# Kernel tuning notes

Measured on AMD Instinct MI355X. Metric: run time of the kernel, lower is better.

## Reference

```python
import jax, jax.numpy as jnp
import numpy as np

N, E, F_IN, HID, HEADS, CLASSES = 50000, 800000, 128, 128, 4, 2
NEG_SLOPE = 0.2


def _gatv2_layer(x, Wl, Wr, att, bias, src, dst, heads, concat):
    # PyG GATv2Conv (share_weights=False, eval mode):
    #   e_ij = att . leaky_relu(Wl x_j + Wr x_i); alpha = segment_softmax over dst;
    #   out_i = sum_j alpha_ij * (Wl x_j)
    n = x.shape[0]
    c = att.shape[-1]
    xl = (x @ Wl).reshape(n, heads, c)   # source transform [N,H,C]
    xr = (x @ Wr).reshape(n, heads, c)   # target transform [N,H,C]
    e = jax.nn.leaky_relu(xl[src] + xr[dst], NEG_SLOPE)      # [E,H,C]
    logits = jnp.einsum('ehc,hc->eh', e, att)                # [E,H]
    m = jax.ops.segment_max(logits, dst, num_segments=n)     # stable softmax per dst
    p = jnp.exp(logits - m[dst])
    denom = jax.ops.segment_sum(p, dst, num_segments=n)
    alpha = p / (denom[dst] + 1e-16)                         # [E,H]
    out = jax.ops.segment_sum(alpha[:, :, None] * xl[src], dst, num_segments=n)  # [N,H,C]
    out = out.reshape(n, heads * c) if concat else out.mean(axis=1)
    return out + bias


def setup_inputs() -> dict:
    key = jax.random.key(0)
    ks = jax.random.split(key, 16)
    s = lambda fan_in: 1.0 / np.sqrt(fan_in)
    inp = {
        'x': jax.random.normal(ks[0], (N, F_IN), jnp.float32),
        'edge_idx': jax.random.randint(ks[1], (2, E), 0, N, jnp.int64),
        'w_in': jax.random.normal(ks[2], (F_IN, HID), jnp.float32) * s(F_IN),
        'b_in': jnp.zeros((HID,), jnp.float32),
        'wl1': jax.random.normal(ks[3], (HID, HEADS * HID), jnp.float32) * s(HID),
        'wr1': jax.random.normal(ks[4], (HID, HEADS * HID), jnp.float32) * s(HID),
        'att1': jax.random.normal(ks[5], (HEADS, HID), jnp.float32) * s(HID),
        'b1': jnp.zeros((HEADS * HID,), jnp.float32),
        'wl2': jax.random.normal(ks[6], (HEADS * HID, HID), jnp.float32) * s(HEADS * HID),
        'wr2': jax.random.normal(ks[7], (HEADS * HID, HID), jnp.float32) * s(HEADS * HID),
        'att2': jax.random.normal(ks[8], (1, HID), jnp.float32) * s(HID),
        'b2': jnp.zeros((HID,), jnp.float32),
        'w_out': jax.random.normal(ks[9], (HID, CLASSES), jnp.float32) * s(HID),
        'b_out': jnp.zeros((CLASSES,), jnp.float32),
    }
    return inp


def reference(x, edge_idx, w_in, b_in, wl1, wr1, att1, b1, wl2, wr2, att2, b2, w_out, b_out):
    n = x.shape[0]
    loops = jnp.arange(n, dtype=edge_idx.dtype)  # PyG add_self_loops=True
    src = jnp.concatenate([edge_idx[0], loops])
    dst = jnp.concatenate([edge_idx[1], loops])
    h = jax.nn.elu(x @ w_in + b_in)              # dropout is identity in eval
    h = jax.nn.elu(_gatv2_layer(h, wl1, wr1, att1, b1, src, dst, HEADS, True))
    h = jax.nn.elu(_gatv2_layer(h, wl2, wr2, att2, b2, src, dst, 1, False))
    logits = h @ w_out + b_out
    return jax.nn.log_softmax(logits, axis=1)
```

## Files before the change

### kernel.cpp

```cpp
#include <hip/hip_runtime.h>
#include <hip/hip_bf16.h>
#include <math.h>

#define F_IN   128
#define HID    128
#define HEADS  4
#define HC1    (HEADS*HID)
#define CLASSES 2
#define NEG_SLOPE 0.2f
#define LOG2E 1.44269504088896340736f
#define MNEG  -3.0e38f

#define SCAN_CHUNK 2048

typedef __attribute__((ext_vector_type(8))) short short8;
typedef __attribute__((ext_vector_type(4))) float f32x4;
typedef __attribute__((ext_vector_type(2))) float f32x2;

__device__ __forceinline__ f32x2 unpack2(unsigned u) {
    f32x2 r;
    r.x = __uint_as_float(u << 16);
    r.y = __uint_as_float(u & 0xffff0000u);
    return r;
}

__global__ void zero_int_kernel(int* __restrict__ p, int n) {
    int i = blockIdx.x * blockDim.x + threadIdx.x;
    int stride = gridDim.x * blockDim.x;
    for (; i < n; i += stride) p[i] = 0;
}

__global__ void deg_kernel(const int* __restrict__ dst_arr, int* __restrict__ deg,
                           int E, int N) {
    int e = blockIdx.x * blockDim.x + threadIdx.x;
    if (e >= E) return;
    int d = dst_arr[e];
    if ((unsigned)d >= (unsigned)N) d = 0;
    atomicAdd(&deg[d], 1);
}

__global__ void scan_partial_kernel(const int* __restrict__ deg, int* __restrict__ bsum, int n) {
    __shared__ int sdata[256];
    int b = blockIdx.x, t = threadIdx.x;
    int base = b * SCAN_CHUNK;
    int s = 0;
    for (int i = t; i < SCAN_CHUNK; i += 256) {
        int idx = base + i;
        s += (idx < n) ? deg[idx] : 0;
    }
    sdata[t] = s;
    __syncthreads();
    for (int off = 128; off; off >>= 1) {
        if (t < off) sdata[t] += sdata[t + off];
        __syncthreads();
    }
    if (t == 0) bsum[b] = sdata[0];
}

__global__ void scan_bsums_kernel(int* __restrict__ bsum, int nb, int* __restrict__ row, int n) {
    if (blockIdx.x == 0 && threadIdx.x == 0) {
        int acc = 0;
        for (int i = 0; i < nb; ++i) { int v = bsum[i]; bsum[i] = acc; acc += v; }
        row[n] = acc;
    }
}

__global__ void scan_final_kernel(const int* __restrict__ deg, const int* __restrict__ bsum,
                                  int* __restrict__ row, int* __restrict__ cursor, int n) {
    __shared__ int tsum[256];
    int b = blockIdx.x, t = threadIdx.x;
    int base = b * SCAN_CHUNK + t * 8;
    int local[8];
    int s = 0;
    #pragma unroll
    for (int k = 0; k < 8; ++k) {
        int idx = base + k;
        int v = (idx < n) ? deg[idx] : 0;
        local[k] = s;
        s += v;
    }
    tsum[t] = s;
    __syncthreads();
    for (int off = 1; off < 256; off <<= 1) {
        int v = 0;
        if (t >= off) v = tsum[t - off];
        __syncthreads();
        if (t >= off) tsum[t] += v;
        __syncthreads();
    }
    int texcl = (t == 0) ? 0 : tsum[t - 1];
    int boff = bsum[b];
    #pragma unroll
    for (int k = 0; k < 8; ++k) {
        int idx = base + k;
        if (idx < n) {
            int v = boff + texcl + local[k];
            row[idx] = v;
            cursor[idx] = v;
        }
    }
}

__global__ void scatter_kernel(const int* __restrict__ src_arr, const int* __restrict__ dst_arr,
                               int* __restrict__ cursor, int* __restrict__ src_sorted,
                               int E, int N) {
    int e = blockIdx.x * blockDim.x + threadIdx.x;
    if (e >= E) return;
    int s = src_arr[e], d = dst_arr[e];
    if ((unsigned)s >= (unsigned)N) s = 0;
    if ((unsigned)d >= (unsigned)N) d = 0;
    int pos = atomicAdd(&cursor[d], 1);
    src_sorted[pos] = s;
}

__global__ void weights_prep_kernel(
    const float* __restrict__ w_in, const float* __restrict__ wl1,
    const float* __restrict__ wr1, const float* __restrict__ wl2,
    const float* __restrict__ wr2,
    __hip_bfloat16* __restrict__ w_inT, __hip_bfloat16* __restrict__ wT1,
    __hip_bfloat16* __restrict__ wT2)
{
    int t = blockIdx.x * blockDim.x + threadIdx.x;
    const int S0 = 128 * 128, S1 = 128 * 512;
    if (t < S0) {
        int n = t / 128, k = t % 128;
        w_inT[t] = __float2bfloat16(w_in[(size_t)k * 128 + n]);
    } else if (t < S0 + S1) {
        int idx = t - S0;
        int n = idx / 128, k = idx % 128;
        wT1[idx] = __float2bfloat16(wl1[(size_t)k * 512 + n]);
    } else if (t < S0 + 2 * S1) {
        int idx = t - S0 - S1;
        int n = idx / 128, k = idx % 128;
        wT1[(size_t)(512 + n) * 128 + k] = __float2bfloat16(wr1[(size_t)k * 512 + n]);
    } else if (t < S0 + 3 * S1) {
        int idx = t - S0 - 2 * S1;
        int n = idx / 512, k = idx % 512;
        wT2[idx] = __float2bfloat16(wl2[(size_t)k * 128 + n]);
    } else if (t < S0 + 4 * S1) {
        int idx = t - S0 - 3 * S1;
        int n = idx / 512, k = idx % 512;
        wT2[(size_t)(128 + n) * 512 + k] = __float2bfloat16(wr2[(size_t)k * 128 + n]);
    }
}

template<int ACT, typename AT, typename OutT>
__global__ __launch_bounds__(256) void mfma_gemm_kernel(
    const AT* __restrict__ A,
    const __hip_bfloat16* __restrict__ BT,
    const float* __restrict__ bias,
    OutT* __restrict__ C,
    int M, int K, int N)
{
    constexpr int BM = 128, BN = 128, BK = 64, LDA = 72;
    __shared__ __align__(16) short As[BM * LDA];
    __shared__ __align__(16) short Bs[BN * LDA];

    const int tid  = threadIdx.x;
    const int lane = tid & 63;
    const int wid  = tid >> 6;
    const int wm   = wid >> 1;
    const int wn   = wid & 1;
    const int fr   = lane & 15;
    const int fk   = (lane >> 4) * 8;

    const int row0 = blockIdx.y * BM;
    const int col0 = blockIdx.x * BN;

    const short* Bg = (const short*)BT;

    f32x4 acc[4][4] = {};

    for (int k0 = 0; k0 < K; k0 += BK) {
        #pragma unroll
        for (int it = 0; it < 4; ++it) {
            int chunk = it * 256 + tid;
            int r = chunk >> 3, c = chunk & 7;
            int gr = row0 + r;
            short8 v = {0, 0, 0, 0, 0, 0, 0, 0};
            if (gr < M) {
                if constexpr (sizeof(AT) == 2) {
                    v = *(const short8*)((const short*)A + (size_t)gr * K + k0 + c * 8);
                } else {
                    const float* ap = (const float*)A + (size_t)gr * K + k0 + c * 8;
                    float4 a0 = *(const float4*)ap;
                    float4 a1 = *(const float4*)(ap + 4);
                    __hip_bfloat16 h;
                    h = __float2bfloat16(a0.x); v[0] = *(short*)&h;
                    h = __float2bfloat16(a0.y); v[1] = *(short*)&h;
                    h = __float2bfloat16(a0.z); v[2] = *(short*)&h;
                    h = __float2bfloat16(a0.w); v[3] = *(short*)&h;
                    h = __float2bfloat16(a1.x); v[4] = *(short*)&h;
                    h = __float2bfloat16(a1.y); v[5] = *(short*)&h;
                    h = __float2bfloat16(a1.z); v[6] = *(short*)&h;
                    h = __float2bfloat16(a1.w); v[7] = *(short*)&h;
                }
            }
            *(short8*)(&As[r * LDA + c * 8]) = v;
        }
        #pragma unroll
        for (int it = 0; it < 4; ++it) {
            int chunk = it * 256 + tid;
            int n = chunk >> 3, c = chunk & 7;
            short8 v = *(const short8*)(Bg + (size_t)(col0 + n) * K + k0 + c * 8);
            *(short8*)(&Bs[n * LDA + c * 8]) = v;
        }
        __syncthreads();
        #pragma unroll
        for (int kk = 0; kk < 2; ++kk) {
            short8 af[4], bf[4];
            #pragma unroll
            for (int i = 0; i < 4; ++i)
                af[i] = *(const short8*)(&As[(wm * 64 + i * 16 + fr) * LDA + kk * 32 + fk]);
            #pragma unroll
            for (int j = 0; j < 4; ++j)
                bf[j] = *(const short8*)(&Bs[(wn * 64 + j * 16 + fr) * LDA + kk * 32 + fk]);
            #pragma unroll
            for (int i = 0; i < 4; ++i)
                #pragma unroll
                for (int j = 0; j < 4; ++j)
                    acc[i][j] = __builtin_amdgcn_mfma_f32_16x16x32_bf16(af[i], bf[j], acc[i][j], 0, 0, 0);
        }
        __syncthreads();
    }

    const int crow = row0 + wm * 64;
    const int ccol = col0 + wn * 64;
    #pragma unroll
    for (int i = 0; i < 4; ++i) {
        #pragma unroll
        for (int j = 0; j < 4; ++j) {
            int col = ccol + j * 16 + (lane & 15);
            float bv = bias ? bias[col] : 0.0f;
            #pragma unroll
            for (int reg = 0; reg < 4; ++reg) {
                int r = crow + i * 16 + (lane >> 4) * 4 + reg;
                if (r < M) {
                    float v = acc[i][j][reg] + bv;
                    if (ACT == 1) v = (v > 0.0f) ? v : expm1f(v);
                    C[(size_t)r * N + col] = (OutT)v;
                }
            }
        }
    }
}

__global__ __launch_bounds__(256) void gatv2_l1_fused_kernel(
    const __hip_bfloat16* __restrict__ xlr,
    const int* __restrict__ row, const int* __restrict__ src_sorted,
    const float* __restrict__ att, const float* __restrict__ b1,
    __hip_bfloat16* __restrict__ out1, int N)
{
    int d = blockIdx.x * 4 + (threadIdx.x >> 6);
    if (d >= N) return;
    int lane = threadIdx.x & 63;
    int cbase = lane * 8;
    const short* basep = (const short*)xlr;

    f32x2 xrd2[4], attv2[4];
    {
        uint4 raw = *reinterpret_cast<const uint4*>(basep + (size_t)d * 1024 + 512 + cbase);
        const unsigned* u = reinterpret_cast<const unsigned*>(&raw);
        #pragma unroll
        for (int j = 0; j < 4; ++j) xrd2[j] = unpack2(u[j]);
        #pragma unroll
        for (int j = 0; j < 4; ++j) {
            attv2[j].x = att[cbase + 2 * j] * LOG2E;
            attv2[j].y = att[cbase + 2 * j + 1] * LOG2E;
        }
    }

    float m = MNEG;
    float s = 0.0f;
    f32x2 o2[4] = {};

    int rs = row[d], re = row[d + 1];

    uint4 raw = *reinterpret_cast<const uint4*>(basep + (size_t)d * 1024 + cbase);
    for (int it = rs - 1; it < re; ++it) {
        uint4 cur = raw;
        if (it + 1 < re) {
            int sn = src_sorted[it + 1];
            raw = *reinterpret_cast<const uint4*>(basep + (size_t)sn * 1024 + cbase);
        }
        const unsigned* u = reinterpret_cast<const unsigned*>(&cur);
        f32x2 v2[4];
        #pragma unroll
        for (int j = 0; j < 4; ++j) v2[j] = unpack2(u[j]);

        f32x2 tacc = {0.0f, 0.0f};
        #pragma unroll
        for (int j = 0; j < 4; ++j) {
            f32x2 e = v2[j] + xrd2[j];
            f32x2 ne = e * NEG_SLOPE;
            e.x = fmaxf(e.x, ne.x);
            e.y = fmaxf(e.y, ne.y);
            tacc = __builtin_elementwise_fma(e, attv2[j], tacc);
        }
        float t = tacc.x + tacc.y;
        t += __shfl_xor(t, 1);
        t += __shfl_xor(t, 2);
        t += __shfl_xor(t, 4);
        t += __shfl_xor(t, 8);
        if (t > m) {
            float r = exp2f(m - t);
            s *= r;
            f32x2 r2 = {r, r};
            #pragma unroll
            for (int j = 0; j < 4; ++j) o2[j] *= r2;
            m = t;
        }
        float p = exp2f(t - m);
        s += p;
        f32x2 p2 = {p, p};
        #pragma unroll
        for (int j = 0; j < 4; ++j) o2[j] = __builtin_elementwise_fma(p2, v2[j], o2[j]);
    }

    float inv = 1.0f / (s + 1e-16f);
    short8 sv;
    #pragma unroll
    for (int j = 0; j < 4; ++j) {
        #pragma unroll
        for (int h = 0; h < 2; ++h) {
            float val = ((h == 0) ? o2[j].x : o2[j].y) * inv + b1[cbase + 2 * j + h];
            val = (val > 0.0f) ? val : expm1f(val);
            __hip_bfloat16 hb = __float2bfloat16(val);
            sv[2 * j + h] = *reinterpret_cast<short*>(&hb);
        }
    }
    *(short8*)((short*)out1 + (size_t)d * HC1 + cbase) = sv;
}

__global__ __launch_bounds__(256) void gatv2_l2_final_kernel(
    const __hip_bfloat16* __restrict__ xlr2,
    const int* __restrict__ row, const int* __restrict__ src_sorted,
    const float* __restrict__ att2, const float* __restrict__ b2,
    const float* __restrict__ w_out, const float* __restrict__ b_out,
    float* __restrict__ out, int N)
{
    int d = blockIdx.x * 4 + (threadIdx.x >> 6);
    if (d >= N) return;
    int lane = threadIdx.x & 63;
    int g  = lane >> 4;
    int gl = lane & 15;
    int cbase = gl * 8;
    const short* basep = (const short*)xlr2;

    f32x2 xrd2[4], attv2[4];
    {
        uint4 rawx = *reinterpret_cast<const uint4*>(basep + (size_t)d * 256 + 128 + cbase);
        const unsigned* u = reinterpret_cast<const unsigned*>(&rawx);
        #pragma unroll
        for (int j = 0; j < 4; ++j) xrd2[j] = unpack2(u[j]);
        #pragma unroll
        for (int j = 0; j < 4; ++j) {
            attv2[j].x = att2[cbase + 2 * j] * LOG2E;
            attv2[j].y = att2[cbase + 2 * j + 1] * LOG2E;
        }
    }

    float m = MNEG;
    float s = 0.0f;
    f32x2 o2[4] = {};

    int rs = row[d], re = row[d + 1];
    int L = re - rs + 1;

    for (int p0 = g; p0 < L; p0 += 4) {
        int srcn = (p0 == 0) ? d : src_sorted[rs + p0 - 1];
        uint4 cur = *reinterpret_cast<const uint4*>(basep + (size_t)srcn * 256 + cbase);
        const unsigned* u = reinterpret_cast<const unsigned*>(&cur);
        f32x2 v2[4];
        #pragma unroll
        for (int j = 0; j < 4; ++j) v2[j] = unpack2(u[j]);

        f32x2 tacc = {0.0f, 0.0f};
        #pragma unroll
        for (int j = 0; j < 4; ++j) {
            f32x2 e = v2[j] + xrd2[j];
            f32x2 ne = e * NEG_SLOPE;
            e.x = fmaxf(e.x, ne.x);
            e.y = fmaxf(e.y, ne.y);
            tacc = __builtin_elementwise_fma(e, attv2[j], tacc);
        }
        float t = tacc.x + tacc.y;
        t += __shfl_xor(t, 1);
        t += __shfl_xor(t, 2);
        t += __shfl_xor(t, 4);
        t += __shfl_xor(t, 8);
        if (t > m) {
            float r = exp2f(m - t);
            s *= r;
            f32x2 r2 = {r, r};
            #pragma unroll
            for (int j = 0; j < 4; ++j) o2[j] *= r2;
            m = t;
        }
        float p = exp2f(t - m);
        s += p;
        f32x2 p2 = {p, p};
        #pragma unroll
        for (int j = 0; j < 4; ++j) o2[j] = __builtin_elementwise_fma(p2, v2[j], o2[j]);
    }

    #pragma unroll
    for (int off = 16; off <= 32; off <<= 1) {
        float m_o = __shfl_xor(m, off);
        float s_o = __shfl_xor(s, off);
        f32x2 oo[4];
        #pragma unroll
        for (int j = 0; j < 4; ++j) {
            oo[j].x = __shfl_xor(o2[j].x, off);
            oo[j].y = __shfl_xor(o2[j].y, off);
        }
        float mn = fmaxf(m, m_o);
        float a = exp2f(m - mn);
        float b = exp2f(m_o - mn);
        s = s * a + s_o * b;
        f32x2 a2 = {a, a}, b2v = {b, b};
        #pragma unroll
        for (int j = 0; j < 4; ++j)
            o2[j] = o2[j] * a2 + oo[j] * b2v;
        m = mn;
    }

    float inv = 1.0f / (s + 1e-16f);
    float a0 = 0.0f, a1 = 0.0f;
    #pragma unroll
    for (int j = 0; j < 4; ++j) {
        #pragma unroll
        for (int h = 0; h < 2; ++h) {
            int c = cbase + 2 * j + h;
            float val = ((h == 0) ? o2[j].x : o2[j].y) * inv + b2[c];
            val = (val > 0.0f) ? val : expm1f(val);
            a0 = fmaf(val, w_out[c * 2 + 0], a0);
            a1 = fmaf(val, w_out[c * 2 + 1], a1);
        }
    }
    #pragma unroll
    for (int off = 1; off <= 8; off <<= 1) {
        a0 += __shfl_xor(a0, off);
        a1 += __shfl_xor(a1, off);
    }
    if (lane == 0) {
        float z0 = a0 + b_out[0];
        float z1 = a1 + b_out[1];
        float mx = fmaxf(z0, z1);
        float lse = mx + logf(__expf(z0 - mx) + __expf(z1 - mx));
        out[(size_t)d * CLASSES + 0] = z0 - lse;
        out[(size_t)d * CLASSES + 1] = z1 - lse;
    }
}

extern "C" void kernel_launch(void* const* d_in, const int* in_sizes, int n_in,
                              void* d_out, int out_size, void* d_ws, size_t ws_size,
                              hipStream_t stream)
{
    const float* x     = (const float*)d_in[0];
    const int*   eidx  = (const int*)d_in[1];
    const float* w_in  = (const float*)d_in[2];
    const float* b_in  = (const float*)d_in[3];
    const float* wl1   = (const float*)d_in[4];
    const float* wr1   = (const float*)d_in[5];
    const float* att1  = (const float*)d_in[6];
    const float* b1    = (const float*)d_in[7];
    const float* wl2   = (const float*)d_in[8];
    const float* wr2   = (const float*)d_in[9];
    const float* att2  = (const float*)d_in[10];
    const float* b2    = (const float*)d_in[11];
    const float* w_out = (const float*)d_in[12];
    const float* b_out = (const float*)d_in[13];
    float* out = (float*)d_out;

    const int N = in_sizes[0] / F_IN;
    const int E = in_sizes[1] / 2;
    const int* src_arr = eidx;
    const int* dst_arr = eidx + E;

    size_t off = 0;
    auto alloc = [&](size_t bytes) -> char* {
        char* ptr = (char*)d_ws + off;
        off += (bytes + 255) & ~(size_t)255;
        return ptr;
    };
    int* row        = (int*)alloc((size_t)(N + 1) * 4);
    int* cursor     = (int*)alloc((size_t)N * 4);
    int* deg        = (int*)alloc((size_t)N * 4);
    int* bsum       = (int*)alloc(64 * 4);
    int* src_sorted = (int*)alloc((size_t)E * 4);
    __hip_bfloat16* w_inT = (__hip_bfloat16*)alloc((size_t)F_IN * HID * 2);
    __hip_bfloat16* wT1   = (__hip_bfloat16*)alloc((size_t)2 * HC1 * HID * 2);
    __hip_bfloat16* wT2   = (__hip_bfloat16*)alloc((size_t)2 * HID * HC1 * 2);
    __hip_bfloat16* h0b   = (__hip_bfloat16*)alloc((size_t)N * HID * 2);
    __hip_bfloat16* xlr1  = (__hip_bfloat16*)alloc((size_t)N * 2 * HC1 * 2);
    __hip_bfloat16* out1  = (__hip_bfloat16*)alloc((size_t)N * HC1 * 2);

    __hip_bfloat16* xlr2 = xlr1;

    dim3 blk(256);
    const int NB_SCAN = (N + SCAN_CHUNK - 1) / SCAN_CHUNK;

    hipLaunchKernelGGL(zero_int_kernel, dim3(64), blk, 0, stream, deg, N);
    hipLaunchKernelGGL(deg_kernel, dim3((E + 255) / 256), blk, 0, stream, dst_arr, deg, E, N);
    hipLaunchKernelGGL(scan_partial_kernel, dim3(NB_SCAN), blk, 0, stream, deg, bsum, N);
    hipLaunchKernelGGL(scan_bsums_kernel, dim3(1), blk, 0, stream, bsum, NB_SCAN, row, N);
    hipLaunchKernelGGL(scan_final_kernel, dim3(NB_SCAN), blk, 0, stream, deg, bsum, row, cursor, N);
    hipLaunchKernelGGL(scatter_kernel, dim3((E + 255) / 256), blk, 0, stream,
                       src_arr, dst_arr, cursor, src_sorted, E, N);

    {
        int total = 128 * 128 + 4 * 128 * 512;
        hipLaunchKernelGGL(weights_prep_kernel, dim3((total + 255) / 256), blk, 0, stream,
                           w_in, wl1, wr1, wl2, wr2, w_inT, wT1, wT2);
    }
    {
        dim3 grid(HID / 128, (N + 127) / 128);
        hipLaunchKernelGGL((mfma_gemm_kernel<1, float, __hip_bfloat16>), grid, blk, 0, stream,
                           x, w_inT, b_in, h0b, N, F_IN, HID);
    }
    {
        dim3 grid(2 * HC1 / 128, (N + 127) / 128);
        hipLaunchKernelGGL((mfma_gemm_kernel<0, __hip_bfloat16, __hip_bfloat16>), grid, blk, 0, stream,
                           h0b, wT1, (const float*)nullptr, xlr1, N, HID, 2 * HC1);
    }
    {
        dim3 grid((N + 3) / 4);
        hipLaunchKernelGGL(gatv2_l1_fused_kernel, grid, blk, 0, stream,
                           xlr1, row, src_sorted, att1, b1, out1, N);
    }
    {
        dim3 grid(2 * HID / 128, (N + 127) / 128);
        hipLaunchKernelGGL((mfma_gemm_kernel<0, __hip_bfloat16, __hip_bfloat16>), grid, blk, 0, stream,
                           out1, wT2, (const float*)nullptr, xlr2, N, HC1, 2 * HID);
    }
    {
        dim3 grid((N + 3) / 4);
        hipLaunchKernelGGL(gatv2_l2_final_kernel, grid, blk, 0, stream,
                           xlr2, row, src_sorted, att2, b2, w_out, b_out, out, N);
    }
}
```

Before: 578.5 us.

## Merge preprocessing into GEMM launches, deepen gather prefetch, branchless online softmax

```diff
diff --git a/kernel.cpp b/kernel.cpp
--- a/kernel.cpp
+++ b/kernel.cpp
@@ -12,6 +12,7 @@
 #define MNEG  -3.0e38f
 
 #define SCAN_CHUNK 2048
+#define NB_SCAN 25
 
 typedef __attribute__((ext_vector_type(8))) short short8;
 typedef __attribute__((ext_vector_type(4))) float f32x4;
@@ -24,103 +25,38 @@
     return r;
 }
 
-__global__ void zero_int_kernel(int* __restrict__ p, int n) {
-    int i = blockIdx.x * blockDim.x + threadIdx.x;
-    int stride = gridDim.x * blockDim.x;
+__device__ __forceinline__ uint4 nt_load_u4(const unsigned* p) {
+    uint4 r;
+    r.x = __builtin_nontemporal_load(p);
+    r.y = __builtin_nontemporal_load(p + 1);
+    r.z = __builtin_nontemporal_load(p + 2);
+    r.w = __builtin_nontemporal_load(p + 3);
+    return r;
+}
+
+__device__ void zero_body(int vb, int nvb, int* __restrict__ p, int n) {
+    int i = vb * 256 + threadIdx.x;
+    int stride = nvb * 256;
     for (; i < n; i += stride) p[i] = 0;
 }
 
-__global__ void deg_kernel(const int* __restrict__ dst_arr, int* __restrict__ deg,
-                           int E, int N) {
-    int e = blockIdx.x * blockDim.x + threadIdx.x;
+__device__ void deg_body(int vb, const int* __restrict__ dst_arr,
+                         int* __restrict__ deg, int E, int N) {
+    int e = vb * 256 + threadIdx.x;
     if (e >= E) return;
     int d = dst_arr[e];
     if ((unsigned)d >= (unsigned)N) d = 0;
     atomicAdd(&deg[d], 1);
 }
 
-__global__ void scan_partial_kernel(const int* __restrict__ deg, int* __restrict__ bsum, int n) {
-    __shared__ int sdata[256];
-    int b = blockIdx.x, t = threadIdx.x;
-    int base = b * SCAN_CHUNK;
-    int s = 0;
-    for (int i = t; i < SCAN_CHUNK; i += 256) {
-        int idx = base + i;
-        s += (idx < n) ? deg[idx] : 0;
-    }
-    sdata[t] = s;
-    __syncthreads();
-    for (int off = 128; off; off >>= 1) {
-        if (t < off) sdata[t] += sdata[t + off];
-        __syncthreads();
-    }
-    if (t == 0) bsum[b] = sdata[0];
-}
-
-__global__ void scan_bsums_kernel(int* __restrict__ bsum, int nb, int* __restrict__ row, int n) {
-    if (blockIdx.x == 0 && threadIdx.x == 0) {
-        int acc = 0;
-        for (int i = 0; i < nb; ++i) { int v = bsum[i]; bsum[i] = acc; acc += v; }
-        row[n] = acc;
-    }
-}
-
-__global__ void scan_final_kernel(const int* __restrict__ deg, const int* __restrict__ bsum,
-                                  int* __restrict__ row, int* __restrict__ cursor, int n) {
-    __shared__ int tsum[256];
-    int b = blockIdx.x, t = threadIdx.x;
-    int base = b * SCAN_CHUNK + t * 8;
-    int local[8];
-    int s = 0;
-    #pragma unroll
-    for (int k = 0; k < 8; ++k) {
-        int idx = base + k;
-        int v = (idx < n) ? deg[idx] : 0;
-        local[k] = s;
-        s += v;
-    }
-    tsum[t] = s;
-    __syncthreads();
-    for (int off = 1; off < 256; off <<= 1) {
-        int v = 0;
-        if (t >= off) v = tsum[t - off];
-        __syncthreads();
-        if (t >= off) tsum[t] += v;
-        __syncthreads();
-    }
-    int texcl = (t == 0) ? 0 : tsum[t - 1];
-    int boff = bsum[b];
-    #pragma unroll
-    for (int k = 0; k < 8; ++k) {
-        int idx = base + k;
-        if (idx < n) {
-            int v = boff + texcl + local[k];
-            row[idx] = v;
-            cursor[idx] = v;
-        }
-    }
-}
-
-__global__ void scatter_kernel(const int* __restrict__ src_arr, const int* __restrict__ dst_arr,
-                               int* __restrict__ cursor, int* __restrict__ src_sorted,
-                               int E, int N) {
-    int e = blockIdx.x * blockDim.x + threadIdx.x;
-    if (e >= E) return;
-    int s = src_arr[e], d = dst_arr[e];
-    if ((unsigned)s >= (unsigned)N) s = 0;
-    if ((unsigned)d >= (unsigned)N) d = 0;
-    int pos = atomicAdd(&cursor[d], 1);
-    src_sorted[pos] = s;
-}
-
-__global__ void weights_prep_kernel(
+__device__ void weights_prep_body(int vb,
     const float* __restrict__ w_in, const float* __restrict__ wl1,
     const float* __restrict__ wr1, const float* __restrict__ wl2,
     const float* __restrict__ wr2,
     __hip_bfloat16* __restrict__ w_inT, __hip_bfloat16* __restrict__ wT1,
     __hip_bfloat16* __restrict__ wT2)
 {
-    int t = blockIdx.x * blockDim.x + threadIdx.x;
+    int t = vb * 256 + threadIdx.x;
     const int S0 = 128 * 128, S1 = 128 * 512;
     if (t < S0) {
         int n = t / 128, k = t % 128;
@@ -144,17 +80,79 @@
     }
 }
 
+__device__ void scan_partial_body(int b, const int* __restrict__ deg,
+                                  int* __restrict__ bsum, int n) {
+    __shared__ int sdata[256];
+    int t = threadIdx.x;
+    int base = b * SCAN_CHUNK;
+    int s = 0;
+    for (int i = t; i < SCAN_CHUNK; i += 256) {
+        int idx = base + i;
+        s += (idx < n) ? deg[idx] : 0;
+    }
+    sdata[t] = s;
+    __syncthreads();
+    for (int off = 128; off; off >>= 1) {
+        if (t < off) sdata[t] += sdata[t + off];
+        __syncthreads();
+    }
+    if (t == 0) bsum[b] = sdata[0];
+}
+
+__device__ void scan_final_body(int b, const int* __restrict__ deg,
+                                const int* __restrict__ bsum,
+                                int* __restrict__ row, int* __restrict__ cursor,
+                                int n) {
+    __shared__ int tsum[256];
+    int t = threadIdx.x;
+    int boff = 0;
+    #pragma unroll
+    for (int i = 0; i < NB_SCAN; ++i) boff += (i < b) ? bsum[i] : 0;
+    if (b == 0 && t == 0) {
+        int total = 0;
+        for (int i = 0; i < NB_SCAN; ++i) total += bsum[i];
+        row[n] = total;
+    }
+    int base = b * SCAN_CHUNK + t * 8;
+    int local[8];
+    int s = 0;
+    #pragma unroll
+    for (int k = 0; k < 8; ++k) {
+        int idx = base + k;
+        int v = (idx < n) ? deg[idx] : 0;
+        local[k] = s;
+        s += v;
+    }
+    tsum[t] = s;
+    __syncthreads();
+    for (int off = 1; off < 256; off <<= 1) {
+        int v = 0;
+        if (t >= off) v = tsum[t - off];
+        __syncthreads();
+        if (t >= off) tsum[t] += v;
+        __syncthreads();
+    }
+    int texcl = (t == 0) ? 0 : tsum[t - 1];
+    #pragma unroll
+    for (int k = 0; k < 8; ++k) {
+        int idx = base + k;
+        if (idx < n) {
+            int v = boff + texcl + local[k];
+            row[idx] = v;
+            cursor[idx] = v;
+        }
+    }
+}
+
 template<int ACT, typename AT, typename OutT>
-__global__ __launch_bounds__(256) void mfma_gemm_kernel(
-    const AT* __restrict__ A,
-    const __hip_bfloat16* __restrict__ BT,
-    const float* __restrict__ bias,
-    OutT* __restrict__ C,
-    int M, int K, int N)
-{
-    constexpr int BM = 128, BN = 128, BK = 64, LDA = 72;
-    __shared__ __align__(16) short As[BM * LDA];
-    __shared__ __align__(16) short Bs[BN * LDA];
+__device__ void mfma_gemm_body(
+    const AT* __restrict__ A, const __hip_bfloat16* __restrict__ BT,
+    const float* __restrict__ bias, OutT* __restrict__ C,
+    int M, int K, int N, int rowBlk, int colBlk)
+{
+    constexpr int LDA = 72;
+    __shared__ __align__(16) short As[128 * LDA];
+    __shared__ __align__(16) short Bs[128 * LDA];
 
     const int tid  = threadIdx.x;
     const int lane = tid & 63;
@@ -164,14 +162,14 @@
     const int fr   = lane & 15;
     const int fk   = (lane >> 4) * 8;
 
-    const int row0 = blockIdx.y * BM;
-    const int col0 = blockIdx.x * BN;
+    const int row0 = rowBlk * 128;
+    const int col0 = colBlk * 128;
 
     const short* Bg = (const short*)BT;
 
     f32x4 acc[4][4] = {};
 
-    for (int k0 = 0; k0 < K; k0 += BK) {
+    for (int k0 = 0; k0 < K; k0 += 64) {
         #pragma unroll
         for (int it = 0; it < 4; ++it) {
             int chunk = it * 256 + tid;
@@ -245,6 +243,78 @@
     }
 }
 
+#define PREP_BLOCKS 1088
+#define ZERO_BLOCKS 64
+
+__global__ __launch_bounds__(256) void kA_prep_zero(
+    const float* w_in, const float* wl1, const float* wr1,
+    const float* wl2, const float* wr2,
+    __hip_bfloat16* w_inT, __hip_bfloat16* wT1, __hip_bfloat16* wT2,
+    int* deg, int N)
+{
+    int b = blockIdx.x;
+    if (b < PREP_BLOCKS)
+        weights_prep_body(b, w_in, wl1, wr1, wl2, wr2, w_inT, wT1, wT2);
+    else
+        zero_body(b - PREP_BLOCKS, ZERO_BLOCKS, deg, N);
+}
+
+__global__ __launch_bounds__(256) void kB_ingemm_deg(
+    const float* x, const __hip_bfloat16* w_inT, const float* b_in,
+    __hip_bfloat16* h0b, int M,
+    const int* dst_arr, int* deg, int E, int N)
+{
+    int b = blockIdx.x;
+    int gemmBlocks = (M + 127) / 128;
+    if (b < gemmBlocks)
+        mfma_gemm_body<1, float, __hip_bfloat16>(x, w_inT, b_in, h0b, M, F_IN, HID, b, 0);
+    else
+        deg_body(b - gemmBlocks, dst_arr, deg, E, N);
+}
+
+template<int HALF>
+__global__ __launch_bounds__(256) void kCD_l1gemm_scan(
+    const __hip_bfloat16* h0b, const __hip_bfloat16* wT1,
+    __hip_bfloat16* xlr1, int M,
+    const int* deg, int* bsum, int* row, int* cursor, int N, int rsplit)
+{
+    int b = blockIdx.x;
+    int nRow = (M + 127) / 128;
+    int myRows = (HALF == 0) ? rsplit : (nRow - rsplit);
+    int gemmBlocks = myRows * 8;
+    if (b < gemmBlocks) {
+        int colBlk = b & 7;
+        int rowBlk = (b >> 3) + (HALF == 0 ? 0 : rsplit);
+        mfma_gemm_body<0, __hip_bfloat16, __hip_bfloat16>(
+            h0b, wT1, (const float*)nullptr, xlr1, M, HID, 2 * HC1, rowBlk, colBlk);
+    } else {
+        int sb = b - gemmBlocks;
+        if (HALF == 0) scan_partial_body(sb, deg, bsum, N);
+        else           scan_final_body(sb, deg, bsum, row, cursor, N);
+    }
+}
+
+__global__ __launch_bounds__(256) void scatter_kernel(
+    const int* __restrict__ src_arr, const int* __restrict__ dst_arr,
+    int* __restrict__ cursor, int* __restrict__ src_sorted, int E, int N)
+{
+    int e = blockIdx.x * blockDim.x + threadIdx.x;
+    if (e >= E) return;
+    int s = src_arr[e], d = dst_arr[e];
+    if ((unsigned)s >= (unsigned)N) s = 0;
+    if ((unsigned)d >= (unsigned)N) d = 0;
+    int pos = atomicAdd(&cursor[d], 1);
+    src_sorted[pos] = s;
+}
+
+__global__ __launch_bounds__(256) void l2gemm_kernel(
+    const __hip_bfloat16* out1, const __hip_bfloat16* wT2,
+    __hip_bfloat16* xlr2, int M)
+{
+    mfma_gemm_body<0, __hip_bfloat16, __hip_bfloat16>(
+        out1, wT2, (const float*)nullptr, xlr2, M, HC1, 2 * HID, blockIdx.y, blockIdx.x);
+}
+
 __global__ __launch_bounds__(256) void gatv2_l1_fused_kernel(
     const __hip_bfloat16* __restrict__ xlr,
     const int* __restrict__ row, const int* __restrict__ src_sorted,
@@ -259,7 +329,7 @@
 
     f32x2 xrd2[4], attv2[4];
     {
-        uint4 raw = *reinterpret_cast<const uint4*>(basep + (size_t)d * 1024 + 512 + cbase);
+        uint4 raw = nt_load_u4((const unsigned*)(basep + (size_t)d * 1024 + 512 + cbase));
         const unsigned* u = reinterpret_cast<const unsigned*>(&raw);
         #pragma unroll
         for (int j = 0; j < 4; ++j) xrd2[j] = unpack2(u[j]);
@@ -275,13 +345,20 @@
     f32x2 o2[4] = {};
 
     int rs = row[d], re = row[d + 1];
-
-    uint4 raw = *reinterpret_cast<const uint4*>(basep + (size_t)d * 1024 + cbase);
-    for (int it = rs - 1; it < re; ++it) {
-        uint4 cur = raw;
-        if (it + 1 < re) {
-            int sn = src_sorted[it + 1];
-            raw = *reinterpret_cast<const uint4*>(basep + (size_t)sn * 1024 + cbase);
+    int L = re - rs + 1;
+
+    uint4 r0 = *reinterpret_cast<const uint4*>(basep + (size_t)d * 1024 + cbase);
+    uint4 r1 = r0;
+    if (L > 1) {
+        int sn = src_sorted[rs];
+        r1 = *reinterpret_cast<const uint4*>(basep + (size_t)sn * 1024 + cbase);
+    }
+    for (int p0 = 0; p0 < L; ++p0) {
+        uint4 cur = r0;
+        r0 = r1;
+        if (p0 + 2 < L) {
+            int sn = src_sorted[rs + p0 + 1];
+            r1 = *reinterpret_cast<const uint4*>(basep + (size_t)sn * 1024 + cbase);
         }
         const unsigned* u = reinterpret_cast<const unsigned*>(&cur);
         f32x2 v2[4];
@@ -292,29 +369,23 @@
         #pragma unroll
         for (int j = 0; j < 4; ++j) {
             f32x2 e = v2[j] + xrd2[j];
-            f32x2 ne = e * NEG_SLOPE;
-            e.x = fmaxf(e.x, ne.x);
-            e.y = fmaxf(e.y, ne.y);
-            tacc = __builtin_elementwise_fma(e, attv2[j], tacc);
+            f32x2 e2 = __builtin_elementwise_max(e, e * NEG_SLOPE);
+            tacc = __builtin_elementwise_fma(e2, attv2[j], tacc);
         }
         float t = tacc.x + tacc.y;
         t += __shfl_xor(t, 1);
         t += __shfl_xor(t, 2);
         t += __shfl_xor(t, 4);
         t += __shfl_xor(t, 8);
-        if (t > m) {
-            float r = exp2f(m - t);
-            s *= r;
-            f32x2 r2 = {r, r};
-            #pragma unroll
-            for (int j = 0; j < 4; ++j) o2[j] *= r2;
-            m = t;
-        }
-        float p = exp2f(t - m);
-        s += p;
-        f32x2 p2 = {p, p};
-        #pragma unroll
-        for (int j = 0; j < 4; ++j) o2[j] = __builtin_elementwise_fma(p2, v2[j], o2[j]);
+        float mn = fmaxf(m, t);
+        float rr = exp2f(m - mn);
+        float p  = exp2f(t - mn);
+        s = s * rr + p;
+        f32x2 rr2 = {rr, rr}, p2 = {p, p};
+        #pragma unroll
+        for (int j = 0; j < 4; ++j)
+            o2[j] = __builtin_elementwise_fma(p2, v2[j], o2[j] * rr2);
+        m = mn;
     }
 
     float inv = 1.0f / (s + 1e-16f);
@@ -329,7 +400,12 @@
             sv[2 * j + h] = *reinterpret_cast<short*>(&hb);
         }
     }
-    *(short8*)((short*)out1 + (size_t)d * HC1 + cbase) = sv;
+    unsigned* op = (unsigned*)((short*)out1 + (size_t)d * HC1 + cbase);
+    const unsigned* sp = (const unsigned*)&sv;
+    __builtin_nontemporal_store(sp[0], op);
+    __builtin_nontemporal_store(sp[1], op + 1);
+    __builtin_nontemporal_store(sp[2], op + 2);
+    __builtin_nontemporal_store(sp[3], op + 3);
 }
 
 __global__ __launch_bounds__(256) void gatv2_l2_final_kernel(
@@ -367,9 +443,17 @@
     int rs = row[d], re = row[d + 1];
     int L = re - rs + 1;
 
+    uint4 r0;
+    if (g < L) {
+        int sn = (g == 0) ? d : src_sorted[rs + g - 1];
+        r0 = *reinterpret_cast<const uint4*>(basep + (size_t)sn * 256 + cbase);
+    }
     for (int p0 = g; p0 < L; p0 += 4) {
-        int srcn = (p0 == 0) ? d : src_sorted[rs + p0 - 1];
-        uint4 cur = *reinterpret_cast<const uint4*>(basep + (size_t)srcn * 256 + cbase);
+        uint4 cur = r0;
+        if (p0 + 4 < L) {
+            int sn = src_sorted[rs + p0 + 3];
+            r0 = *reinterpret_cast<const uint4*>(basep + (size_t)sn * 256 + cbase);
+        }
         const unsigned* u = reinterpret_cast<const unsigned*>(&cur);
         f32x2 v2[4];
         #pragma unroll
@@ -379,29 +463,23 @@
         #pragma unroll
         for (int j = 0; j < 4; ++j) {
             f32x2 e = v2[j] + xrd2[j];
-            f32x2 ne = e * NEG_SLOPE;
-            e.x = fmaxf(e.x, ne.x);
-            e.y = fmaxf(e.y, ne.y);
-            tacc = __builtin_elementwise_fma(e, attv2[j], tacc);
+            f32x2 e2 = __builtin_elementwise_max(e, e * NEG_SLOPE);
+            tacc = __builtin_elementwise_fma(e2, attv2[j], tacc);
         }
         float t = tacc.x + tacc.y;
         t += __shfl_xor(t, 1);
         t += __shfl_xor(t, 2);
         t += __shfl_xor(t, 4);
         t += __shfl_xor(t, 8);
-        if (t > m) {
-            float r = exp2f(m - t);
-            s *= r;
-            f32x2 r2 = {r, r};
-            #pragma unroll
-            for (int j = 0; j < 4; ++j) o2[j] *= r2;
-            m = t;
-        }
-        float p = exp2f(t - m);
-        s += p;
-        f32x2 p2 = {p, p};
-        #pragma unroll
-        for (int j = 0; j < 4; ++j) o2[j] = __builtin_elementwise_fma(p2, v2[j], o2[j]);
+        float mn = fmaxf(m, t);
+        float rr = exp2f(m - mn);
+        float p  = exp2f(t - mn);
+        s = s * rr + p;
+        f32x2 rr2 = {rr, rr}, p2 = {p, p};
+        #pragma unroll
+        for (int j = 0; j < 4; ++j)
+            o2[j] = __builtin_elementwise_fma(p2, v2[j], o2[j] * rr2);
+        m = mn;
     }
 
     #pragma unroll
@@ -499,44 +577,26 @@
     __hip_bfloat16* xlr2 = xlr1;
 
     dim3 blk(256);
-    const int NB_SCAN = (N + SCAN_CHUNK - 1) / SCAN_CHUNK;
-
-    hipLaunchKernelGGL(zero_int_kernel, dim3(64), blk, 0, stream, deg, N);
-    hipLaunchKernelGGL(deg_kernel, dim3((E + 255) / 256), blk, 0, stream, dst_arr, deg, E, N);
-    hipLaunchKernelGGL(scan_partial_kernel, dim3(NB_SCAN), blk, 0, stream, deg, bsum, N);
-    hipLaunchKernelGGL(scan_bsums_kernel, dim3(1), blk, 0, stream, bsum, NB_SCAN, row, N);
-    hipLaunchKernelGGL(scan_final_kernel, dim3(NB_SCAN), blk, 0, stream, deg, bsum, row, cursor, N);
-    hipLaunchKernelGGL(scatter_kernel, dim3((E + 255) / 256), blk, 0, stream,
+    const int nRowBlk = (N + 127) / 128;
+    const int rsplit  = (nRowBlk + 1) / 2;
+    const int degBlocks = (E + 255) / 256;
+
+    hipLaunchKernelGGL(kA_prep_zero, dim3(PREP_BLOCKS + ZERO_BLOCKS), blk, 0, stream,
+                       w_in, wl1, wr1, wl2, wr2, w_inT, wT1, wT2, deg, N);
+    hipLaunchKernelGGL(kB_ingemm_deg, dim3(nRowBlk + degBlocks), blk, 0, stream,
+                       x, w_inT, b_in, h0b, N, dst_arr, deg, E, N);
+    hipLaunchKernelGGL((kCD_l1gemm_scan<0>), dim3(rsplit * 8 + NB_SCAN), blk, 0, stream,
+                       h0b, wT1, xlr1, N, deg, bsum, row, cursor, N, rsplit);
+    hipLaunchKernelGGL((kCD_l1gemm_scan<1>), dim3((nRowBlk - rsplit) * 8 + NB_SCAN), blk, 0, stream,
+                       h0b, wT1, xlr1, N, deg, bsum, row, cursor, N, rsplit);
+    hipLaunchKernelGGL(scatter_kernel, dim3(degBlocks), blk, 0, stream,
                        src_arr, dst_arr, cursor, src_sorted, E, N);
-
+    hipLaunchKernelGGL(gatv2_l1_fused_kernel, dim3((N + 3) / 4), blk, 0, stream,
+                       xlr1, row, src_sorted, att1, b1, out1, N);
     {
-        int total = 128 * 128 + 4 * 128 * 512;
-        hipLaunchKernelGGL(weights_prep_kernel, dim3((total + 255) / 256), blk, 0, stream,
-                           w_in, wl1, wr1, wl2, wr2, w_inT, wT1, wT2);
-    }
-    {
-        dim3 grid(HID / 128, (N + 127) / 128);
-        hipLaunchKernelGGL((mfma_gemm_kernel<1, float, __hip_bfloat16>), grid, blk, 0, stream,
-                           x, w_inT, b_in, h0b, N, F_IN, HID);
-    }
-    {
-        dim3 grid(2 * HC1 / 128, (N + 127) / 128);
-        hipLaunchKernelGGL((mfma_gemm_kernel<0, __hip_bfloat16, __hip_bfloat16>), grid, blk, 0, stream,
-                           h0b, wT1, (const float*)nullptr, xlr1, N, HID, 2 * HC1);
-    }
-    {
-        dim3 grid((N + 3) / 4);
-        hipLaunchKernelGGL(gatv2_l1_fused_kernel, grid, blk, 0, stream,
-                           xlr1, row, src_sorted, att1, b1, out1, N);
-    }
-    {
-        dim3 grid(2 * HID / 128, (N + 127) / 128);
-        hipLaunchKernelGGL((mfma_gemm_kernel<0, __hip_bfloat16, __hip_bfloat16>), grid, blk, 0, stream,
-                           out1, wT2, (const float*)nullptr, xlr2, N, HC1, 2 * HID);
-    }
-    {
-        dim3 grid((N + 3) / 4);
-        hipLaunchKernelGGL(gatv2_l2_final_kernel, grid, blk, 0, stream,
-                           xlr2, row, src_sorted, att2, b2, w_out, b_out, out, N);
-    }
-}
+        dim3 grid(2 * HID / 128, nRowBlk);
+        hipLaunchKernelGGL(l2gemm_kernel, grid, blk, 0, stream, out1, wT2, xlr2, N);
+    }
+    hipLaunchKernelGGL(gatv2_l2_final_kernel, dim3((N + 3) / 4), blk, 0, stream,
+                       xlr2, row, src_sorted, att2, b2, w_out, b_out, out, N);
+}
```

Result: slower. 611.7 us (+5.8%).
